# Optimization experiments

Measured on AMD Instinct MI355X. Metric: run time of the kernel, lower is better.

Reference implementation:

```python
import jax, jax.numpy as jnp
import numpy as np

N_NODES = 100000
N_EDGES = 1600000
D_IN = 128
D_HID = 128
D_OUT = 16
N_LAYERS = 3
N_GRAPHS = 64
EPS = 1e-12


def _glorot(key, shape):
    fan_in = shape[-1]
    bound = 1.0 / np.sqrt(fan_in)
    return jax.random.uniform(key, shape, jnp.float32, -bound, bound)


def setup_inputs() -> dict:
    key = jax.random.key(0)
    ks = jax.random.split(key, 12)
    x = jax.random.normal(ks[0], (N_NODES, D_IN), jnp.float32)
    edge_index = jax.random.randint(ks[1], (2, N_EDGES), 0, N_NODES, jnp.int64)
    batch = jnp.sort(jax.random.randint(ks[2], (N_NODES,), 0, N_GRAPHS, jnp.int64))
    # stacked GraphSage weights: torch Linear stores [out, in]
    Wl = _glorot(ks[3], (N_LAYERS, D_HID, D_IN))
    bl = _glorot(ks[4], (N_LAYERS, D_HID))
    Wr = _glorot(ks[5], (N_LAYERS, D_HID, D_IN))
    br = _glorot(ks[6], (N_LAYERS, D_HID))
    W1 = _glorot(ks[7], (D_HID, D_HID))
    b1 = _glorot(ks[8], (D_HID,))
    W2 = _glorot(ks[9], (D_OUT, D_HID))
    b2 = _glorot(ks[10], (D_OUT,))
    return {"x": x, "edge_index": edge_index, "batch": batch,
            "Wl": Wl, "bl": bl, "Wr": Wr, "br": br,
            "W1": W1, "b1": b1, "W2": W2, "b2": b2}


def reference(x, edge_index, batch, Wl, bl, Wr, br, W1, b1, W2, b2):
    N = x.shape[0]
    src, dst = edge_index[0], edge_index[1]
    # in-degree for mean aggregation (clamped to avoid div-by-zero)
    deg = jax.ops.segment_sum(jnp.ones_like(dst, dtype=x.dtype), dst, num_segments=N)
    deg = jnp.maximum(deg, 1.0)[:, None]
    h = x
    for i in range(N_LAYERS):
        # lin_r applied at nodes, then gathered (equivalent to lin_r(x_j) per edge)
        hr = h @ Wr[i].T + br[i]
        msg = hr[src]                               # [E, D_HID] gather
        agg = jax.ops.segment_sum(msg, dst, num_segments=N) / deg  # scatter-mean
        out = agg + (h @ Wl[i].T + bl[i])
        # F.normalize(out) -> L2 norm along dim=1, eps=1e-12
        nrm = jnp.maximum(jnp.linalg.norm(out, axis=1, keepdims=True), EPS)
        h = jax.nn.relu(out / nrm)                  # dropout is identity (eval)
    # post message-passing MLP (dropout identity in eval mode)
    h = h @ W1.T + b1
    h = h @ W2.T + b2
    # global mean pool over graphs
    cnt = jnp.maximum(jax.ops.segment_sum(jnp.ones_like(batch, dtype=h.dtype), batch, num_segments=N_GRAPHS), 1.0)
    pooled = jax.ops.segment_sum(h, batch, num_segments=N_GRAPHS) / cnt[:, None]
    return jax.nn.log_softmax(pooled, axis=1)
```

## Files before the change

### kernel.cpp

```cpp
#include <hip/hip_runtime.h>
#include <cstdint>
#include <cstddef>

#define NN 100000
#define NE 1600000
#define DD 128
#define NG 64
#define NB 782
#define GB 1563

#if defined(__has_builtin)
#if __has_builtin(__builtin_amdgcn_cvt_pk_f32_fp8) && __has_builtin(__builtin_amdgcn_cvt_pk_fp8_f32)
#define USE_FP8 1
#endif
#endif
#ifndef USE_FP8
#define USE_FP8 0
#endif

using bf16x8 = __attribute__((ext_vector_type(8))) short;
using f32x4  = __attribute__((ext_vector_type(4))) float;
using f32x2  = __attribute__((ext_vector_type(2))) float;

__device__ __forceinline__ int clampi(int v, int hi) {
    v = v < 0 ? 0 : v;
    return v >= hi ? hi - 1 : v;
}
__device__ __forceinline__ unsigned short f2bf(float f) {
    unsigned int u = __float_as_uint(f);
    u += 0x7fffu + ((u >> 16) & 1u);
    return (unsigned short)(u >> 16);
}
__device__ __forceinline__ float bf2f(unsigned short s) {
    return __uint_as_float(((unsigned int)s) << 16);
}
#if USE_FP8
__device__ __forceinline__ unsigned char f2fp8(float v) {
    return (unsigned char)(__builtin_amdgcn_cvt_pk_fp8_f32(v, 0.f, 0, false) & 0xFF);
}
#endif

#define WTOT (3 * 256 * 128)
__global__ void cvtw_kernel(const float* __restrict__ Wl, const float* __restrict__ Wr,
                            unsigned short* __restrict__ Wcat3,
                            int* __restrict__ bcnt, int* __restrict__ gcur0,
                            float* __restrict__ pooled, float* __restrict__ cnt) {
    int t = blockIdx.x * 256 + threadIdx.x;
    if (t < NB) { bcnt[t] = 0; gcur0[t] = 0; }
    if (t < NG * DD) pooled[t] = 0.f;
    if (t < NG) cnt[t] = 0.f;
    if (t < WTOT) {
        int j    = t & 7;
        int lane = (t >> 3) & 63;
        int ks   = (t >> 9) & 3;
        int n    = (t >> 11) & 7;
        int half = (t >> 14) & 1;
        int l    = t >> 15;
        int l15 = lane & 15, lg = lane >> 4;
        int o = n * 16 + l15;
        int k = ks * 32 + lg * 8 + j;
        const float* Wsrc = half ? Wr : Wl;
        Wcat3[t] = f2bf(Wsrc[(size_t)l * 16384 + o * 128 + k]);
    }
}

template <bool F32IN>
__global__ __launch_bounds__(256) void gemm4_kernel(
    const void* __restrict__ hin_, const unsigned short* __restrict__ Wf,
    const float* __restrict__ bl, unsigned short* __restrict__ zb,
    unsigned char* __restrict__ ub, const int* __restrict__ dst,
    int* __restrict__ bcnt, int nG) {
    __shared__ unsigned short lA[64 * 128];
    __shared__ unsigned short sstz[64][136];

    if (blockIdx.x >= nG) {
        int* lcnt = (int*)lA;
        for (int i = threadIdx.x; i < NB; i += 256) lcnt[i] = 0;
        __syncthreads();
        int b = blockIdx.x - nG;
        int e0 = b * 8000;
        int e1 = e0 + 8000; if (e1 > NE) e1 = NE;
        for (int e = e0 + threadIdx.x; e < e1; e += 256)
            atomicAdd(&lcnt[clampi(dst[e], NN) >> 7], 1);
        __syncthreads();
        for (int i = threadIdx.x; i < NB; i += 256)
            if (lcnt[i]) atomicAdd(&bcnt[i], lcnt[i]);
        return;
    }

    const int tid = threadIdx.x;
    const int w = tid >> 6, l = tid & 63;
    const int l15 = l & 15, lg = l >> 4;
    const int n0 = blockIdx.x * 64;

#pragma unroll
    for (int q = 0; q < 4; ++q) {
        int d = (q * 256 + tid) * 16;
        int row = d >> 8;
        int colb = d & 255;
        int srow = n0 + row; srow = srow < NN ? srow : NN - 1;
        bf16x8 v;
        if (F32IN) {
            const float* rp = (const float*)hin_ + (size_t)srow * DD + (colb >> 1);
            const float4 f0 = *(const float4*)rp;
            const float4 f1 = *(const float4*)(rp + 4);
            v[0] = (short)f2bf(f0.x); v[1] = (short)f2bf(f0.y);
            v[2] = (short)f2bf(f0.z); v[3] = (short)f2bf(f0.w);
            v[4] = (short)f2bf(f1.x); v[5] = (short)f2bf(f1.y);
            v[6] = (short)f2bf(f1.z); v[7] = (short)f2bf(f1.w);
        } else {
            v = *(const bf16x8*)((const unsigned short*)hin_ + (size_t)srow * DD + (colb >> 1));
        }
        int sd = d ^ (((d >> 8) & 7) << 4);
        *(bf16x8*)((char*)lA + sd) = v;
    }
    __syncthreads();

    const int half = w >> 1, rt = w & 1;

    bf16x8 a[4][2];
#pragma unroll
    for (int ks = 0; ks < 4; ++ks)
#pragma unroll
        for (int m = 0; m < 2; ++m) {
            int row = rt * 32 + m * 16 + l15;
            int L = row * 256 + ks * 64 + lg * 16;
            int SL = L ^ (((L >> 8) & 7) << 4);
            a[ks][m] = *(const bf16x8*)((char*)lA + SL);
        }

    f32x4 acc[2][8];
#pragma unroll
    for (int m = 0; m < 2; ++m)
#pragma unroll
        for (int n = 0; n < 8; ++n) acc[m][n] = (f32x4){0.f, 0.f, 0.f, 0.f};

    const unsigned short* Wb = Wf + ((size_t)half << 14);
#pragma unroll
    for (int ks = 0; ks < 4; ++ks) {
#pragma unroll
        for (int n = 0; n < 8; ++n) {
            bf16x8 b = *(const bf16x8*)(Wb + (((n << 2) + ks) << 9) + (l << 3));
            acc[0][n] = __builtin_amdgcn_mfma_f32_16x16x32_bf16(a[ks][0], b, acc[0][n], 0, 0, 0);
            acc[1][n] = __builtin_amdgcn_mfma_f32_16x16x32_bf16(a[ks][1], b, acc[1][n], 0, 0, 0);
        }
    }

    __syncthreads();

    if (half == 0) {
        float blv[8];
#pragma unroll
        for (int n = 0; n < 8; ++n) blv[n] = bl[n * 16 + l15];
#pragma unroll
        for (int m = 0; m < 2; ++m)
#pragma unroll
            for (int r = 0; r < 4; ++r) {
                int brow = rt * 32 + m * 16 + lg * 4 + r;
#pragma unroll
                for (int n = 0; n < 8; ++n)
                    sstz[brow][n * 16 + l15] = f2bf(acc[m][n][r] + blv[n]);
            }
#pragma unroll
        for (int p = 0; p < 8; ++p) {
            int brow = rt * 32 + p * 4 + lg;
            int node = n0 + brow;
            bf16x8 vv = *(const bf16x8*)(&sstz[brow][l15 * 8]);
            if (node < NN)
                *(bf16x8*)(zb + (size_t)node * DD + l15 * 8) = vv;
        }
    } else {
#if USE_FP8
        unsigned char* sstu = (unsigned char*)lA;
#pragma unroll
        for (int m = 0; m < 2; ++m)
#pragma unroll
            for (int r = 0; r < 4; ++r) {
                int brow = rt * 32 + m * 16 + lg * 4 + r;
#pragma unroll
                for (int n = 0; n < 8; ++n)
                    sstu[brow * 136 + n * 16 + l15] = f2fp8(acc[m][n][r]);
            }
        __builtin_amdgcn_s_waitcnt(0);
#pragma unroll
        for (int p = 0; p < 8; ++p) {
            int brow = rt * 32 + p * 4 + lg;
            int node = n0 + brow;
            uint2 vv = *(const uint2*)(sstu + brow * 136 + l15 * 8);
            if (node < NN)
                *(uint2*)(ub + (size_t)node * DD + l15 * 8) = vv;
        }
#else
        unsigned short* ub16 = (unsigned short*)ub;
#pragma unroll
        for (int m = 0; m < 2; ++m)
#pragma unroll
            for (int r = 0; r < 4; ++r) {
                int brow = rt * 32 + m * 16 + lg * 4 + r;
                int node = n0 + brow;
                if (node < NN)
#pragma unroll
                    for (int n = 0; n < 8; ++n)
                        ub16[(size_t)node * DD + n * 16 + l15] = f2bf(acc[m][n][r]);
            }
#endif
    }
}

__global__ __launch_bounds__(256) void bpart2_kernel(
    const int* __restrict__ src, const int* __restrict__ dst,
    const int* __restrict__ bcnt, int* __restrict__ gcur0,
    int* __restrict__ bstart_g, uint2* __restrict__ stage) {
    __shared__ int bst[NB];
    __shared__ int lcnt[NB];
    __shared__ int partial[256];
    const int t = threadIdx.x;
    int own[4]; int ssum = 0;
#pragma unroll
    for (int q = 0; q < 4; ++q) {
        int idx = t * 4 + q;
        own[q] = (idx < NB) ? bcnt[idx] : 0;
        ssum += own[q];
    }
    partial[t] = ssum;
    __syncthreads();
    for (int d = 1; d < 256; d <<= 1) {
        int v = (t >= d) ? partial[t - d] : 0;
        __syncthreads();
        partial[t] += v;
        __syncthreads();
    }
    int run = partial[t] - ssum;
#pragma unroll
    for (int q = 0; q < 4; ++q) {
        int idx = t * 4 + q;
        if (idx < NB) bst[idx] = run;
        run += own[q];
    }
    if (blockIdx.x == 0) {
#pragma unroll
        for (int q = 0; q < 4; ++q) {
            int idx = t * 4 + q;
            if (idx < NB) bstart_g[idx] = bst[idx];
        }
        if (t == 0) bstart_g[NB] = NE;
    }
    for (int i = t; i < NB; i += 256) lcnt[i] = 0;
    __syncthreads();
    int e0 = blockIdx.x * 8000;
    int e1 = e0 + 8000; if (e1 > NE) e1 = NE;
    for (int e = e0 + t; e < e1; e += 256)
        atomicAdd(&lcnt[clampi(dst[e], NN) >> 7], 1);
    __syncthreads();
    for (int i = t; i < NB; i += 256) {
        int c = lcnt[i];
        if (c) lcnt[i] = bst[i] + atomicAdd(&gcur0[i], c);
    }
    __syncthreads();
    for (int e = e0 + t; e < e1; e += 256) {
        int d = clampi(dst[e], NN);
        int pos = atomicAdd(&lcnt[d >> 7], 1);
        uint2 p; p.x = (unsigned)clampi(src[e], NN); p.y = (unsigned)d;
        stage[pos] = p;
    }
}

__global__ __launch_bounds__(256) void bfill_kernel(
    const uint2* __restrict__ stage, const int* __restrict__ bstart,
    int* __restrict__ row_ptr, int* __restrict__ csr) {
    __shared__ int scnt[128];
    __shared__ int scur[128];
    const int b = blockIdx.x;
    const int t = threadIdx.x;
    const int s0 = bstart[b], s1 = bstart[b + 1];
    const int n0 = b << 7;
    int nend = NN - n0; if (nend > 128) nend = 128;
    if (t < 128) scnt[t] = 0;
    __syncthreads();
    for (int i = s0 + t; i < s1; i += 256)
        atomicAdd(&scnt[stage[i].y & 127], 1);
    __syncthreads();
    int own = (t < 128) ? scnt[t] : 0;
    for (int d = 1; d < 128; d <<= 1) {
        int v = (t < 128 && t >= d) ? scnt[t - d] : 0;
        __syncthreads();
        if (t < 128) scnt[t] += v;
        __syncthreads();
    }
    if (t < 128) {
        int excl = scnt[t] - own;
        scur[t] = excl;
        if (t < nend) row_ptr[n0 + t] = s0 + excl;
    }
    if (b == NB - 1 && t == 0) row_ptr[NN] = NE;
    __syncthreads();
    for (int i = s0 + t; i < s1; i += 256) {
        uint2 p = stage[i];
        int slot = atomicAdd(&scur[p.y & 127], 1);
        csr[s0 + slot] = (int)p.x;
    }
}

__global__ __launch_bounds__(256) void pullc8_kernel(
    const unsigned char* __restrict__ u, const unsigned short* __restrict__ z,
    const float* __restrict__ br, const int* __restrict__ row_ptr,
    const int* __restrict__ csr, unsigned short* __restrict__ hOut) {
    int w = threadIdx.x >> 6, lane = threadIdx.x & 63;
    int n = blockIdx.x * 4 + w;
    if (n >= NN) return;
    int s0 = row_ptr[n], s1 = row_ptr[n + 1];
    int len = s1 - s0;
    float inv = 1.0f / (float)(len > 0 ? len : 1);
#if USE_FP8
    int g8 = lane >> 3, c8 = lane & 7;
    float acc[16];
#pragma unroll
    for (int q = 0; q < 16; ++q) acc[q] = 0.f;
    int j = s0 + g8;
    for (; j + 8 < s1; j += 16) {
        int i0 = csr[j], i1 = csr[j + 8];
        const uint4 v0 = *(const uint4*)(u + (size_t)i0 * DD + c8 * 16);
        const uint4 v1 = *(const uint4*)(u + (size_t)i1 * DD + c8 * 16);
#pragma unroll
        for (int dwi = 0; dwi < 4; ++dwi) {
            unsigned a0 = (&v0.x)[dwi], a1 = (&v1.x)[dwi];
            f32x2 p;
            p = __builtin_amdgcn_cvt_pk_f32_fp8(a0, false); acc[dwi*4+0] += p.x; acc[dwi*4+1] += p.y;
            p = __builtin_amdgcn_cvt_pk_f32_fp8(a0, true);  acc[dwi*4+2] += p.x; acc[dwi*4+3] += p.y;
            p = __builtin_amdgcn_cvt_pk_f32_fp8(a1, false); acc[dwi*4+0] += p.x; acc[dwi*4+1] += p.y;
            p = __builtin_amdgcn_cvt_pk_f32_fp8(a1, true);  acc[dwi*4+2] += p.x; acc[dwi*4+3] += p.y;
        }
    }
    for (; j < s1; j += 8) {
        int i0 = csr[j];
        const uint4 v0 = *(const uint4*)(u + (size_t)i0 * DD + c8 * 16);
#pragma unroll
        for (int dwi = 0; dwi < 4; ++dwi) {
            unsigned a0 = (&v0.x)[dwi];
            f32x2 p;
            p = __builtin_amdgcn_cvt_pk_f32_fp8(a0, false); acc[dwi*4+0] += p.x; acc[dwi*4+1] += p.y;
            p = __builtin_amdgcn_cvt_pk_f32_fp8(a0, true);  acc[dwi*4+2] += p.x; acc[dwi*4+3] += p.y;
        }
    }
#pragma unroll
    for (int q = 0; q < 16; ++q) {
        acc[q] += __shfl_xor(acc[q], 8);
        acc[q] += __shfl_xor(acc[q], 16);
        acc[q] += __shfl_xor(acc[q], 32);
    }
    const bf16x8 zv0 = *(const bf16x8*)(z + (size_t)n * DD + c8 * 16);
    const bf16x8 zv1 = *(const bf16x8*)(z + (size_t)n * DD + c8 * 16 + 8);
    float bg = len > 0 ? 1.f : 0.f;
    float v[16]; float ss = 0.f;
#pragma unroll
    for (int q = 0; q < 16; ++q) {
        unsigned short zz = (unsigned short)(q < 8 ? zv0[q] : zv1[q - 8]);
        v[q] = acc[q] * inv + bf2f(zz) + bg * br[c8 * 16 + q];
        ss = fmaf(v[q], v[q], ss);
    }
    ss += __shfl_xor(ss, 1); ss += __shfl_xor(ss, 2); ss += __shfl_xor(ss, 4);
    float invn = 1.0f / fmaxf(sqrtf(ss), 1e-12f);
    if (g8 == 0) {
        bf16x8 r0, r1;
#pragma unroll
        for (int q = 0; q < 8; ++q) {
            r0[q] = (short)f2bf(fmaxf(v[q], 0.f) * invn);
            r1[q] = (short)f2bf(fmaxf(v[q + 8], 0.f) * invn);
        }
        *(bf16x8*)(hOut + (size_t)n * DD + c8 * 16) = r0;
        *(bf16x8*)(hOut + (size_t)n * DD + c8 * 16 + 8) = r1;
    }
#else
    int g = lane >> 4, c = lane & 15;
    const unsigned short* ub16 = (const unsigned short*)u;
    float acc[8];
#pragma unroll
    for (int q = 0; q < 8; ++q) acc[q] = 0.f;
    for (int j = s0 + g; j < s1; j += 4) {
        bf16x8 v0 = *(const bf16x8*)(ub16 + (size_t)csr[j] * DD + c * 8);
#pragma unroll
        for (int q = 0; q < 8; ++q) acc[q] += bf2f((unsigned short)v0[q]);
    }
#pragma unroll
    for (int q = 0; q < 8; ++q) {
        acc[q] += __shfl_xor(acc[q], 16);
        acc[q] += __shfl_xor(acc[q], 32);
    }
    bf16x8 zv = *(const bf16x8*)(z + (size_t)n * DD + c * 8);
    float bg = len > 0 ? 1.f : 0.f;
    float v[8]; float ss = 0.f;
#pragma unroll
    for (int q = 0; q < 8; ++q) {
        v[q] = acc[q] * inv + bf2f((unsigned short)zv[q]) + bg * br[c * 8 + q];
        ss = fmaf(v[q], v[q], ss);
    }
    ss += __shfl_xor(ss, 1); ss += __shfl_xor(ss, 2);
    ss += __shfl_xor(ss, 4); ss += __shfl_xor(ss, 8);
    float invn = 1.0f / fmaxf(sqrtf(ss), 1e-12f);
    if (g == 0) {
        bf16x8 r;
#pragma unroll
        for (int q = 0; q < 8; ++q) r[q] = (short)f2bf(fmaxf(v[q], 0.f) * invn);
        *(bf16x8*)(hOut + (size_t)n * DD + c * 8) = r;
    }
#endif
}

__global__ __launch_bounds__(256) void pool_bf16(
    const unsigned short* __restrict__ h, const int* __restrict__ batch,
    float* __restrict__ pooled, float* __restrict__ cnt) {
    int hw = (blockIdx.x * blockDim.x + threadIdx.x) >> 5;
    int lane = threadIdx.x & 31;
    int total_hw = (gridDim.x * blockDim.x) >> 5;
    int chunk = (NN + total_hw - 1) / total_hw;
    int nbeg = hw * chunk;
    int nend = nbeg + chunk; if (nend > NN) nend = NN;
    if (nbeg >= nend) return;
    float ax = 0.f, ay = 0.f, az = 0.f, aw = 0.f;
    int curg = clampi(batch[nbeg], NG);
    int run = 0;
    for (int n = nbeg; n < nend; ++n) {
        int g = clampi(batch[n], NG);
        if (g != curg) {
            atomicAdd(&pooled[curg * DD + lane * 4 + 0], ax);
            atomicAdd(&pooled[curg * DD + lane * 4 + 1], ay);
            atomicAdd(&pooled[curg * DD + lane * 4 + 2], az);
            atomicAdd(&pooled[curg * DD + lane * 4 + 3], aw);
            if (lane == 0) atomicAdd(&cnt[curg], (float)run);
            ax = ay = az = aw = 0.f; run = 0; curg = g;
        }
        const ushort4 v = *(const ushort4*)(h + (size_t)n * DD + lane * 4);
        ax += bf2f(v.x); ay += bf2f(v.y); az += bf2f(v.z); aw += bf2f(v.w);
        ++run;
    }
    atomicAdd(&pooled[curg * DD + lane * 4 + 0], ax);
    atomicAdd(&pooled[curg * DD + lane * 4 + 1], ay);
    atomicAdd(&pooled[curg * DD + lane * 4 + 2], az);
    atomicAdd(&pooled[curg * DD + lane * 4 + 3], aw);
    if (lane == 0) atomicAdd(&cnt[curg], (float)run);
}

__global__ __launch_bounds__(1024) void tail_kernel(
    const float* __restrict__ pooled, const float* __restrict__ cnt,
    const float* __restrict__ W1, const float* __restrict__ b1,
    const float* __restrict__ W2, const float* __restrict__ b2,
    float* __restrict__ out) {
    __shared__ float Wc[16][128];
    __shared__ float bcs[16];
    int t = threadIdx.x;
    for (int i = t; i < 2048; i += 1024) {
        int o = i >> 7, k = i & 127;
        float s = 0.f;
        for (int j = 0; j < 128; ++j) s = fmaf(W2[o * 128 + j], W1[j * 128 + k], s);
        Wc[o][k] = s;
    }
    if (t < 16) {
        float sb = 0.f;
        for (int j = 0; j < 128; ++j) sb = fmaf(W2[t * 128 + j], b1[j], sb);
        bcs[t] = sb + b2[t];
    }
    __syncthreads();
    int g = t >> 4, o = t & 15;
    float invc = 1.0f / fmaxf(cnt[g], 1.0f);
    float z = bcs[o];
    for (int k = 0; k < 128; ++k) z = fmaf(pooled[g * DD + k] * invc, Wc[o][k], z);
    float m = z;
    m = fmaxf(m, __shfl_xor(m, 1)); m = fmaxf(m, __shfl_xor(m, 2));
    m = fmaxf(m, __shfl_xor(m, 4)); m = fmaxf(m, __shfl_xor(m, 8));
    float e = expf(z - m);
    float s = e;
    s += __shfl_xor(s, 1); s += __shfl_xor(s, 2);
    s += __shfl_xor(s, 4); s += __shfl_xor(s, 8);
    out[g * 16 + o] = z - m - logf(s);
}

__global__ void zero_out_kernel(float* __restrict__ out, int n) {
    int i = blockIdx.x * 256 + threadIdx.x;
    if (i < n) out[i] = 0.f;
}

extern "C" void kernel_launch(void* const* d_in, const int* in_sizes, int n_in,
                              void* d_out, int out_size, void* d_ws, size_t ws_size,
                              hipStream_t stream) {
    const float* x  = (const float*)d_in[0];
    const int*   ei = (const int*)d_in[1];
    const int* batch = (const int*)d_in[2];
    const float* Wl = (const float*)d_in[3];
    const float* bl = (const float*)d_in[4];
    const float* Wr = (const float*)d_in[5];
    const float* br = (const float*)d_in[6];
    const float* W1 = (const float*)d_in[7];
    const float* b1 = (const float*)d_in[8];
    const float* W2 = (const float*)d_in[9];
    const float* b2 = (const float*)d_in[10];
    float* out = (float*)d_out;

    const int* src = ei;
    const int* dst = ei + NE;

    char* ws = (char*)d_ws;
    size_t off = 0;
    auto alloc = [&](size_t bytes) -> void* {
        void* p = ws + off; off += (bytes + 255) & ~(size_t)255; return p;
    };
    unsigned short* hA    = (unsigned short*)alloc((size_t)NN * DD * 2);
    unsigned short* hB    = (unsigned short*)alloc((size_t)NN * DD * 2);
    unsigned short* zb    = (unsigned short*)alloc((size_t)NN * DD * 2);
    unsigned char*  ub    = (unsigned char*)alloc((size_t)NN * DD * 2);
    unsigned short* Wcat3 = (unsigned short*)alloc((size_t)WTOT * 2);
    int* row_ptr  = (int*)alloc((size_t)(NN + 1) * 4);
    int* csr      = (int*)alloc((size_t)NE * 4);
    uint2* stage  = (uint2*)alloc((size_t)NE * 8);
    int* bcnt     = (int*)alloc((size_t)NB * 4);
    int* bstart   = (int*)alloc((size_t)(NB + 1) * 4);
    int* gcur0    = (int*)alloc((size_t)NB * 4);
    float* pooled = (float*)alloc(NG * DD * 4);
    float* cnt    = (float*)alloc(NG * 4);

    if (off > ws_size) {
        zero_out_kernel<<<(out_size + 255) / 256, 256, 0, stream>>>(out, out_size);
        return;
    }

    cvtw_kernel<<<(WTOT + 255) / 256, 256, 0, stream>>>(
        Wl, Wr, Wcat3, bcnt, gcur0, pooled, cnt);

    const int npb = (NE + 7999) / 8000;

    gemm4_kernel<true><<<GB + npb, 256, 0, stream>>>(
        x, Wcat3, bl, zb, ub, dst, bcnt, GB);

    bpart2_kernel<<<npb, 256, 0, stream>>>(src, dst, bcnt, gcur0, bstart, stage);
    bfill_kernel<<<NB, 256, 0, stream>>>(stage, bstart, row_ptr, csr);

    unsigned short* bufs[2] = {hA, hB};
    pullc8_kernel<<<(NN + 3) / 4, 256, 0, stream>>>(
        ub, zb, br, row_ptr, csr, bufs[0]);
    const unsigned short* hin = bufs[0];
    for (int l = 1; l < 3; ++l) {
        gemm4_kernel<false><<<GB, 256, 0, stream>>>(
            hin, Wcat3 + (size_t)l * 32768, bl + (size_t)l * 128,
            zb, ub, dst, bcnt, GB);
        pullc8_kernel<<<(NN + 3) / 4, 256, 0, stream>>>(
            ub, zb, br + (size_t)l * 128, row_ptr, csr, bufs[l & 1]);
        hin = bufs[l & 1];
    }

    pool_bf16<<<256, 256, 0, stream>>>(hin, batch, pooled, cnt);
    tail_kernel<<<1, 1024, 0, stream>>>(pooled, cnt, W1, b1, W2, b2, out);
}
```

Before: 387.0 us.

## Process two nodes per wavefront in FP8 gather with interleaved 4-deep loads

Replaces the one-node-per-wave gather kernel with one in which each wavefront aggregates two destination nodes at once. Each 16-lane group reads 8-byte FP8 slices, so the wave covers 4 neighbor rows at a time instead of 8. The main loop issues 8 independent row loads, 4 per node, interleaved across both nodes to raise memory-level parallelism. The grid halves, and bias values are hoisted into registers. It adds loop tails and unequal degree handling between the paired nodes, and each lane now loads 8 bytes per row rather than 16.

```diff
diff --git a/kernel.cpp b/kernel.cpp
--- a/kernel.cpp
+++ b/kernel.cpp
@@ -301,109 +301,155 @@
     }
 }
 
-__global__ __launch_bounds__(256) void pullc8_kernel(
+#if USE_FP8
+__device__ __forceinline__ void acc_row(f32x2* a2, uint2 v) {
+    f32x2 p;
+    p = __builtin_amdgcn_cvt_pk_f32_fp8(v.x, false); a2[0] += p;
+    p = __builtin_amdgcn_cvt_pk_f32_fp8(v.x, true);  a2[1] += p;
+    p = __builtin_amdgcn_cvt_pk_f32_fp8(v.y, false); a2[2] += p;
+    p = __builtin_amdgcn_cvt_pk_f32_fp8(v.y, true);  a2[3] += p;
+}
+#endif
+
+__global__ __launch_bounds__(256) void pullc2_kernel(
     const unsigned char* __restrict__ u, const unsigned short* __restrict__ z,
     const float* __restrict__ br, const int* __restrict__ row_ptr,
     const int* __restrict__ csr, unsigned short* __restrict__ hOut) {
     int w = threadIdx.x >> 6, lane = threadIdx.x & 63;
-    int n = blockIdx.x * 4 + w;
-    if (n >= NN) return;
-    int s0 = row_ptr[n], s1 = row_ptr[n + 1];
-    int len = s1 - s0;
-    float inv = 1.0f / (float)(len > 0 ? len : 1);
+    int g = lane >> 4, c = lane & 15;
+    int nA = blockIdx.x * 8 + w * 2;
+    if (nA >= NN) return;
+    int nB = nA + 1;
+    bool hasB = nB < NN;
+    int s0a = row_ptr[nA], s1a = row_ptr[nA + 1];
+    int s0b = 0, s1b = 0;
+    if (hasB) { s0b = row_ptr[nB], s1b = row_ptr[nB + 1]; }
+    int lenA = s1a - s0a, lenB = s1b - s0b;
+    bf16x8 zvA = *(const bf16x8*)(z + (size_t)nA * DD + c * 8);
+    bf16x8 zvB = *(const bf16x8*)(z + (size_t)(hasB ? nB : nA) * DD + c * 8);
+    float brv[8];
+#pragma unroll
+    for (int q = 0; q < 8; ++q) brv[q] = br[c * 8 + q];
+
 #if USE_FP8
-    int g8 = lane >> 3, c8 = lane & 7;
-    float acc[16];
-#pragma unroll
-    for (int q = 0; q < 16; ++q) acc[q] = 0.f;
-    int j = s0 + g8;
-    for (; j + 8 < s1; j += 16) {
-        int i0 = csr[j], i1 = csr[j + 8];
-        const uint4 v0 = *(const uint4*)(u + (size_t)i0 * DD + c8 * 16);
-        const uint4 v1 = *(const uint4*)(u + (size_t)i1 * DD + c8 * 16);
-#pragma unroll
-        for (int dwi = 0; dwi < 4; ++dwi) {
-            unsigned a0 = (&v0.x)[dwi], a1 = (&v1.x)[dwi];
-            f32x2 p;
-            p = __builtin_amdgcn_cvt_pk_f32_fp8(a0, false); acc[dwi*4+0] += p.x; acc[dwi*4+1] += p.y;
-            p = __builtin_amdgcn_cvt_pk_f32_fp8(a0, true);  acc[dwi*4+2] += p.x; acc[dwi*4+3] += p.y;
-            p = __builtin_amdgcn_cvt_pk_f32_fp8(a1, false); acc[dwi*4+0] += p.x; acc[dwi*4+1] += p.y;
-            p = __builtin_amdgcn_cvt_pk_f32_fp8(a1, true);  acc[dwi*4+2] += p.x; acc[dwi*4+3] += p.y;
-        }
-    }
-    for (; j < s1; j += 8) {
-        int i0 = csr[j];
-        const uint4 v0 = *(const uint4*)(u + (size_t)i0 * DD + c8 * 16);
-#pragma unroll
-        for (int dwi = 0; dwi < 4; ++dwi) {
-            unsigned a0 = (&v0.x)[dwi];
-            f32x2 p;
-            p = __builtin_amdgcn_cvt_pk_f32_fp8(a0, false); acc[dwi*4+0] += p.x; acc[dwi*4+1] += p.y;
-            p = __builtin_amdgcn_cvt_pk_f32_fp8(a0, true);  acc[dwi*4+2] += p.x; acc[dwi*4+3] += p.y;
-        }
-    }
-#pragma unroll
-    for (int q = 0; q < 16; ++q) {
-        acc[q] += __shfl_xor(acc[q], 8);
-        acc[q] += __shfl_xor(acc[q], 16);
-        acc[q] += __shfl_xor(acc[q], 32);
-    }
-    const bf16x8 zv0 = *(const bf16x8*)(z + (size_t)n * DD + c8 * 16);
-    const bf16x8 zv1 = *(const bf16x8*)(z + (size_t)n * DD + c8 * 16 + 8);
-    float bg = len > 0 ? 1.f : 0.f;
-    float v[16]; float ss = 0.f;
-#pragma unroll
-    for (int q = 0; q < 16; ++q) {
-        unsigned short zz = (unsigned short)(q < 8 ? zv0[q] : zv1[q - 8]);
-        v[q] = acc[q] * inv + bf2f(zz) + bg * br[c8 * 16 + q];
-        ss = fmaf(v[q], v[q], ss);
-    }
-    ss += __shfl_xor(ss, 1); ss += __shfl_xor(ss, 2); ss += __shfl_xor(ss, 4);
-    float invn = 1.0f / fmaxf(sqrtf(ss), 1e-12f);
-    if (g8 == 0) {
-        bf16x8 r0, r1;
+    f32x2 aA[4], aB[4];
+#pragma unroll
+    for (int q = 0; q < 4; ++q) { aA[q] = (f32x2){0.f, 0.f}; aB[q] = (f32x2){0.f, 0.f}; }
+    int jA = s0a + g, jB = s0b + g;
+    while (jA + 12 < s1a && jB + 12 < s1b) {
+        int iA0 = csr[jA], iA1 = csr[jA + 4], iA2 = csr[jA + 8], iA3 = csr[jA + 12];
+        int iB0 = csr[jB], iB1 = csr[jB + 4], iB2 = csr[jB + 8], iB3 = csr[jB + 12];
+        uint2 vA0 = *(const uint2*)(u + (size_t)iA0 * DD + c * 8);
+        uint2 vA1 = *(const uint2*)(u + (size_t)iA1 * DD + c * 8);
+        uint2 vA2 = *(const uint2*)(u + (size_t)iA2 * DD + c * 8);
+        uint2 vA3 = *(const uint2*)(u + (size_t)iA3 * DD + c * 8);
+        uint2 vB0 = *(const uint2*)(u + (size_t)iB0 * DD + c * 8);
+        uint2 vB1 = *(const uint2*)(u + (size_t)iB1 * DD + c * 8);
+        uint2 vB2 = *(const uint2*)(u + (size_t)iB2 * DD + c * 8);
+        uint2 vB3 = *(const uint2*)(u + (size_t)iB3 * DD + c * 8);
+        acc_row(aA, vA0); acc_row(aA, vA1); acc_row(aA, vA2); acc_row(aA, vA3);
+        acc_row(aB, vB0); acc_row(aB, vB1); acc_row(aB, vB2); acc_row(aB, vB3);
+        jA += 16; jB += 16;
+    }
+    while (jA + 12 < s1a) {
+        int i0 = csr[jA], i1 = csr[jA + 4], i2 = csr[jA + 8], i3 = csr[jA + 12];
+        uint2 v0 = *(const uint2*)(u + (size_t)i0 * DD + c * 8);
+        uint2 v1 = *(const uint2*)(u + (size_t)i1 * DD + c * 8);
+        uint2 v2 = *(const uint2*)(u + (size_t)i2 * DD + c * 8);
+        uint2 v3 = *(const uint2*)(u + (size_t)i3 * DD + c * 8);
+        acc_row(aA, v0); acc_row(aA, v1); acc_row(aA, v2); acc_row(aA, v3);
+        jA += 16;
+    }
+    while (jB + 12 < s1b) {
+        int i0 = csr[jB], i1 = csr[jB + 4], i2 = csr[jB + 8], i3 = csr[jB + 12];
+        uint2 v0 = *(const uint2*)(u + (size_t)i0 * DD + c * 8);
+        uint2 v1 = *(const uint2*)(u + (size_t)i1 * DD + c * 8);
+        uint2 v2 = *(const uint2*)(u + (size_t)i2 * DD + c * 8);
+        uint2 v3 = *(const uint2*)(u + (size_t)i3 * DD + c * 8);
+        acc_row(aB, v0); acc_row(aB, v1); acc_row(aB, v2); acc_row(aB, v3);
+        jB += 16;
+    }
+    while (jA < s1a && jB < s1b) {
+        uint2 v0 = *(const uint2*)(u + (size_t)csr[jA] * DD + c * 8);
+        uint2 v1 = *(const uint2*)(u + (size_t)csr[jB] * DD + c * 8);
+        acc_row(aA, v0); acc_row(aB, v1);
+        jA += 4; jB += 4;
+    }
+    for (; jA < s1a; jA += 4) {
+        uint2 v0 = *(const uint2*)(u + (size_t)csr[jA] * DD + c * 8);
+        acc_row(aA, v0);
+    }
+    for (; jB < s1b; jB += 4) {
+        uint2 v0 = *(const uint2*)(u + (size_t)csr[jB] * DD + c * 8);
+        acc_row(aB, v0);
+    }
+    float accA[8], accB[8];
+#pragma unroll
+    for (int q = 0; q < 4; ++q) {
+        accA[q * 2] = aA[q].x; accA[q * 2 + 1] = aA[q].y;
+        accB[q * 2] = aB[q].x; accB[q * 2 + 1] = aB[q].y;
+    }
+#else
+    const unsigned short* ub16 = (const unsigned short*)u;
+    float accA[8], accB[8];
+#pragma unroll
+    for (int q = 0; q < 8; ++q) { accA[q] = 0.f; accB[q] = 0.f; }
+    for (int j = s0a + g; j < s1a; j += 4) {
+        bf16x8 v0 = *(const bf16x8*)(ub16 + (size_t)csr[j] * DD + c * 8);
+#pragma unroll
+        for (int q = 0; q < 8; ++q) accA[q] += bf2f((unsigned short)v0[q]);
+    }
+    for (int j = s0b + g; j < s1b; j += 4) {
+        bf16x8 v0 = *(const bf16x8*)(ub16 + (size_t)csr[j] * DD + c * 8);
+#pragma unroll
+        for (int q = 0; q < 8; ++q) accB[q] += bf2f((unsigned short)v0[q]);
+    }
+#endif
+#pragma unroll
+    for (int q = 0; q < 8; ++q) {
+        accA[q] += __shfl_xor(accA[q], 16);
+        accA[q] += __shfl_xor(accA[q], 32);
+        accB[q] += __shfl_xor(accB[q], 16);
+        accB[q] += __shfl_xor(accB[q], 32);
+    }
+    {
+        float inv = 1.0f / (float)(lenA > 0 ? lenA : 1);
+        float bg = lenA > 0 ? 1.f : 0.f;
+        float v[8]; float ss = 0.f;
 #pragma unroll
         for (int q = 0; q < 8; ++q) {
-            r0[q] = (short)f2bf(fmaxf(v[q], 0.f) * invn);
-            r1[q] = (short)f2bf(fmaxf(v[q + 8], 0.f) * invn);
-        }
-        *(bf16x8*)(hOut + (size_t)n * DD + c8 * 16) = r0;
-        *(bf16x8*)(hOut + (size_t)n * DD + c8 * 16 + 8) = r1;
-    }
-#else
-    int g = lane >> 4, c = lane & 15;
-    const unsigned short* ub16 = (const unsigned short*)u;
-    float acc[8];
-#pragma unroll
-    for (int q = 0; q < 8; ++q) acc[q] = 0.f;
-    for (int j = s0 + g; j < s1; j += 4) {
-        bf16x8 v0 = *(const bf16x8*)(ub16 + (size_t)csr[j] * DD + c * 8);
-#pragma unroll
-        for (int q = 0; q < 8; ++q) acc[q] += bf2f((unsigned short)v0[q]);
-    }
-#pragma unroll
-    for (int q = 0; q < 8; ++q) {
-        acc[q] += __shfl_xor(acc[q], 16);
-        acc[q] += __shfl_xor(acc[q], 32);
-    }
-    bf16x8 zv = *(const bf16x8*)(z + (size_t)n * DD + c * 8);
-    float bg = len > 0 ? 1.f : 0.f;
-    float v[8]; float ss = 0.f;
-#pragma unroll
-    for (int q = 0; q < 8; ++q) {
-        v[q] = acc[q] * inv + bf2f((unsigned short)zv[q]) + bg * br[c * 8 + q];
-        ss = fmaf(v[q], v[q], ss);
-    }
-    ss += __shfl_xor(ss, 1); ss += __shfl_xor(ss, 2);
-    ss += __shfl_xor(ss, 4); ss += __shfl_xor(ss, 8);
-    float invn = 1.0f / fmaxf(sqrtf(ss), 1e-12f);
-    if (g == 0) {
-        bf16x8 r;
-#pragma unroll
-        for (int q = 0; q < 8; ++q) r[q] = (short)f2bf(fmaxf(v[q], 0.f) * invn);
-        *(bf16x8*)(hOut + (size_t)n * DD + c * 8) = r;
-    }
-#endif
+            v[q] = accA[q] * inv + bf2f((unsigned short)zvA[q]) + bg * brv[q];
+            ss = fmaf(v[q], v[q], ss);
+        }
+        ss += __shfl_xor(ss, 1); ss += __shfl_xor(ss, 2);
+        ss += __shfl_xor(ss, 4); ss += __shfl_xor(ss, 8);
+        float invn = 1.0f / fmaxf(sqrtf(ss), 1e-12f);
+        if (g == 0) {
+            bf16x8 r;
+#pragma unroll
+            for (int q = 0; q < 8; ++q) r[q] = (short)f2bf(fmaxf(v[q], 0.f) * invn);
+            *(bf16x8*)(hOut + (size_t)nA * DD + c * 8) = r;
+        }
+    }
+    if (hasB) {
+        float inv = 1.0f / (float)(lenB > 0 ? lenB : 1);
+        float bg = lenB > 0 ? 1.f : 0.f;
+        float v[8]; float ss = 0.f;
+#pragma unroll
+        for (int q = 0; q < 8; ++q) {
+            v[q] = accB[q] * inv + bf2f((unsigned short)zvB[q]) + bg * brv[q];
+            ss = fmaf(v[q], v[q], ss);
+        }
+        ss += __shfl_xor(ss, 1); ss += __shfl_xor(ss, 2);
+        ss += __shfl_xor(ss, 4); ss += __shfl_xor(ss, 8);
+        float invn = 1.0f / fmaxf(sqrtf(ss), 1e-12f);
+        if (g == 0) {
+            bf16x8 r;
+#pragma unroll
+            for (int q = 0; q < 8; ++q) r[q] = (short)f2bf(fmaxf(v[q], 0.f) * invn);
+            *(bf16x8*)(hOut + (size_t)nB * DD + c * 8) = r;
+        }
+    }
 }
 
 __global__ __launch_bounds__(256) void pool_bf16(
@@ -534,14 +580,14 @@
     bfill_kernel<<<NB, 256, 0, stream>>>(stage, bstart, row_ptr, csr);
 
     unsigned short* bufs[2] = {hA, hB};
-    pullc8_kernel<<<(NN + 3) / 4, 256, 0, stream>>>(
+    pullc2_kernel<<<(NN + 7) / 8, 256, 0, stream>>>(
         ub, zb, br, row_ptr, csr, bufs[0]);
     const unsigned short* hin = bufs[0];
     for (int l = 1; l < 3; ++l) {
         gemm4_kernel<false><<<GB, 256, 0, stream>>>(
             hin, Wcat3 + (size_t)l * 32768, bl + (size_t)l * 128,
             zb, ub, dst, bcnt, GB);
-        pullc8_kernel<<<(NN + 3) / 4, 256, 0, stream>>>(
+        pullc2_kernel<<<(NN + 7) / 8, 256, 0, stream>>>(
             ub, zb, br + (size_t)l * 128, row_ptr, csr, bufs[l & 1]);
         hin = bufs[l & 1];
     }
```

After: 457.0 us. 18.1% more time.
